# Kernel tuning notes

Measured on AMD Instinct MI355X. Metric: run time of the kernel, lower is better.

## Reference

```python
import jax, jax.numpy as jnp
import numpy as np

EPS = 1e-8
N = 1024          # number of points
C = 16            # channels per layer
RBF_LOW, RBF_HIGH, RBF_COUNT = 0.0, 3.5, 32


def _rand(key, shape, scale=0.1):
    return scale * jax.random.normal(key, shape, dtype=jnp.float32)


def setup_inputs() -> dict:
    key = jax.random.key(0)
    ks = jax.random.split(key, 20)
    R = RBF_COUNT
    return {
        'points':   jax.random.normal(ks[0], (N, 3), dtype=jnp.float32),
        # layer 1: 2 radial filters (0->0 and 0->1), output_dim = 1 input channel
        'l1_W1':    _rand(ks[1],  (2, R, R)),
        'l1_B1':    _rand(ks[2],  (2, R)),
        'l1_W2':    _rand(ks[3],  (2, R, 1)),
        'l1_B2':    _rand(ks[4],  (2, 1)),
        'l1_si0_w': _rand(ks[5],  (C, 1)),
        'l1_si0_b': _rand(ks[6],  (C,)),
        'l1_si1_w': _rand(ks[7],  (C, 1)),
        'l1_nl_b':  _rand(ks[8],  (C,)),
        # layer 2: 5 radial filters (0->0, 0->1, 1->0, 1->1 id, 1->1 levi-civita)
        'l2_W1':    _rand(ks[9],  (5, R, R)),
        'l2_B1':    _rand(ks[10], (5, R)),
        'l2_W2':    _rand(ks[11], (5, R, C)),
        'l2_B2':    _rand(ks[12], (5, C)),
        'l2_si0_w': _rand(ks[13], (C, 2 * C)),
        'l2_si0_b': _rand(ks[14], (C,)),
        'l2_si1_w': _rand(ks[15], (C, 3 * C)),
        'l2_nl_b':  _rand(ks[16], (C,)),
        # readout
        'fc_w':     _rand(ks[17], (C, 8)),
        'fc_b':     _rand(ks[18], (8,)),
    }


def _eijk():
    e = np.zeros((3, 3, 3), dtype=np.float32)
    e[0, 1, 2] = e[1, 2, 0] = e[2, 0, 1] = 1.0
    e[0, 2, 1] = e[2, 1, 0] = e[1, 0, 2] = -1.0
    return jnp.asarray(e)


def _norm_eps(x, axis, keepdims=False):
    # norm_with_epsilon: sqrt(max(sum(x^2), EPS))
    return jnp.sqrt(jnp.maximum(jnp.sum(x * x, axis=axis, keepdims=keepdims), EPS))


def _radial(rbf, w1, b1, w2, b2):
    # R(): two-layer relu MLP on rbf features -> [N, N, F]
    h = jax.nn.relu(rbf @ w1 + b1)
    return h @ w2 + b2


def _geometry(points):
    rij = points[:, None, :] - points[None, :, :]          # [N,N,3]
    ss = jnp.sum(rij * rij, axis=-1)                        # [N,N]
    mask0 = ss < EPS                                        # dij == 0 (diagonal)
    dij = jnp.where(mask0, 0.0, jnp.sqrt(jnp.where(mask0, 1.0, ss)))
    centers = jnp.linspace(RBF_LOW, RBF_HIGH, RBF_COUNT, dtype=jnp.float32)
    gamma = jnp.float32(RBF_COUNT / (RBF_HIGH - RBF_LOW))
    rbf = jnp.exp(-gamma * (dij[..., None] - centers) ** 2)  # [N,N,RBF]
    unit = rij / _norm_eps(rij, axis=-1, keepdims=True)       # unit_vectors
    return rbf, unit, mask0


def _F1(rad, unit, mask0):
    # F_1: mask radial where dij==0, multiply by unit vectors -> [N,N,F,3]
    mr = jnp.where(mask0[..., None], 0.0, rad)
    return mr[..., None] * unit[:, :, None, :]


def _nonlinearity(x0, x1, b1):
    # degree-0: pointwise elu; degree-1: norm nonlinearity x * elu(|x|+b)/|x|
    x0 = jax.nn.elu(x0)
    n = _norm_eps(x1, axis=-1)                              # [N,C]
    x1 = x1 * (jax.nn.elu(n + b1) / n)[..., None]
    return x0, x1


def reference(points, l1_W1, l1_B1, l1_W2, l1_B2, l1_si0_w, l1_si0_b, l1_si1_w,
              l1_nl_b, l2_W1, l2_B1, l2_W2, l2_B2, l2_si0_w, l2_si0_b, l2_si1_w,
              l2_nl_b, fc_w, fc_b):
    rbf, unit, mask0 = _geometry(points)
    eijk = _eijk().astype(points.dtype)
    n_pts = points.shape[0]
    x0 = jnp.ones((n_pts, 1, 1), dtype=points.dtype)        # degree-0 input [N,1,1]

    # ---- layer 1: only degree-0 input -> (0->0) and (0->1) filters ----
    r00 = _radial(rbf, l1_W1[0], l1_B1[0], l1_W2[0], l1_B2[0])
    out0 = jnp.einsum('abf,bfi->afi', r00, x0)              # filter_0
    F1a = _F1(_radial(rbf, l1_W1[1], l1_B1[1], l1_W2[1], l1_B2[1]), unit, mask0)
    out1 = jnp.einsum('abfi,bf->afi', F1a, x0[..., 0])
    x0 = jnp.einsum('afi,gf->agi', out0, l1_si0_w) + l1_si0_b[:, None]
    x1 = jnp.einsum('afi,gf->agi', out1, l1_si1_w)
    x0, x1 = _nonlinearity(x0, x1, l1_nl_b)                 # [N,C,1], [N,C,3]

    # ---- layer 2: degree-0 and degree-1 inputs -> 5 filters ----
    rads = [_radial(rbf, l2_W1[i], l2_B1[i], l2_W2[i], l2_B2[i]) for i in range(5)]
    c00 = jnp.einsum('abf,bfi->afi', rads[0], x0)                          # 0x0->0
    c01 = jnp.einsum('abfi,bf->afi', _F1(rads[1], unit, mask0), x0[..., 0])  # 0x1->1
    c10 = jnp.einsum('abfj,bfj->af', _F1(rads[2], unit, mask0), x1)[..., None]  # 1x1->0
    c11 = jnp.einsum('abf,bfi->afi', rads[3], x1)                          # 1x0->1
    c11x = jnp.einsum('ijk,abfj,bfk->afi', eijk, _F1(rads[4], unit, mask0), x1)  # 1x1->1
    cat0 = jnp.concatenate([c00, c10], axis=-2)             # [N,2C,1]
    cat1 = jnp.concatenate([c01, c11, c11x], axis=-2)       # [N,3C,3]
    x0 = jnp.einsum('afi,gf->agi', cat0, l2_si0_w) + l2_si0_b[:, None]
    x1 = jnp.einsum('afi,gf->agi', cat1, l2_si1_w)
    x0, x1 = _nonlinearity(x0, x1, l2_nl_b)

    # ---- readout: invariant degree-0 features, mean-pool over points ----
    g = jnp.mean(x0[..., 0], axis=0)                        # [C]
    return g @ fc_w + fc_b                                  # [num_classes]
```

## Files before the change

### kernel.cpp

```cpp
#include <hip/hip_runtime.h>
#include <hip/hip_bf16.h>
#include <math.h>

#define NP 1024
#define R 32
#define C 16
#define GAMMA (32.0f/3.5f)
#define DC (3.5f/31.0f)
#define GDC2 (64.0f/31.0f)
#define GDD  (112.0f/961.0f)
#define NBANK 32

typedef __attribute__((ext_vector_type(8))) short bf16x8;
typedef __attribute__((ext_vector_type(4))) float f32x4;

__device__ __forceinline__ short tobf(float x){
    __hip_bfloat16 h = __float2bfloat16(x);
    return __builtin_bit_cast(short, h);
}
__device__ __forceinline__ unsigned pack2bf(float a, float b){
    const unsigned lo = (unsigned short)tobf(a);
    const unsigned hi = (unsigned short)tobf(b);
    return lo | (hi << 16);
}
__device__ __forceinline__ float eluf(float x){ return x > 0.f ? x : expm1f(x); }

__device__ __forceinline__ f32x4 mfma16(bf16x8 a, bf16x8 b, f32x4 c){
    return __builtin_amdgcn_mfma_f32_16x16x32_bf16(a, b, c, 0, 0, 0);
}

template<int STRIDE>
__device__ __forceinline__ void load_bfrag(const float* __restrict__ src, int q, int n,
                                           bf16x8& w){
    #pragma unroll
    for (int jj = 0; jj < 8; jj++)
        w[jj] = tobf(src[(q*8+jj)*STRIDE + n]);
}

__device__ __forceinline__ bf16x8 rbf_frag(float d, float qd8, float c0q, float c1){
    const float t0 = d - qd8;
    float r = __expf(-GAMMA * t0 * t0);
    float M = __expf(GDC2 * d) * c0q;
    bf16x8 afrag;
    afrag[0] = tobf(r);
    #pragma unroll
    for (int jj = 1; jj < 8; jj++){
        r *= M;  M *= c1;
        afrag[jj] = tobf(r);
    }
    return afrag;
}

__global__ __launch_bounds__(256) void k_l1p(
    const float* __restrict__ points,
    const float* __restrict__ W1, const float* __restrict__ B1,
    const float* __restrict__ W2, const float* __restrict__ B2,
    const float* __restrict__ si0w, const float* __restrict__ si0b,
    const float* __restrict__ si1w, const float* __restrict__ nlb,
    float* __restrict__ xall, float* __restrict__ l1c,
    unsigned* __restrict__ cntL1)
{
    __shared__ float sW[4][8];
    __shared__ float sFin[8];
    __shared__ unsigned sAm;

    const int tid  = threadIdx.x;
    const int lane = tid & 63;
    const int wv   = tid >> 6;
    const int l16  = lane & 15;
    const int q    = lane >> 4;
    const int a    = blockIdx.x >> 1;
    const int half = blockIdx.x & 1;
    const float pax = points[a*3+0], pay = points[a*3+1], paz = points[a*3+2];
    const float qd8 = (float)(q*8) * DC;
    const float c0q = __expf(-GDD * (1.0f + 16.0f*(float)q));
    const float c1  = __expf(-2.0f * GDD);

    bf16x8 w1f[2][2];
    float  b1v[2][2], w2s[2], w2t[2];
    #pragma unroll
    for (int fi = 0; fi < 2; fi++)
        #pragma unroll
        for (int nt = 0; nt < 2; nt++){
            load_bfrag<R>(W1 + fi*R*R, q, nt*16 + l16, w1f[fi][nt]);
            b1v[fi][nt] = B1[fi*R + nt*16 + l16];
        }
    #pragma unroll
    for (int nt = 0; nt < 2; nt++){
        w2s[nt] = W2[nt*16 + l16];
        w2t[nt] = W2[R + nt*16 + l16];
    }

    float s0a[2] = {0.f, 0.f};
    float T[2][3] = {};
    float upx = 0.f, upy = 0.f, upz = 0.f;

    for (int bt = half*8; bt < half*8 + 8; bt++){
        const int bA = bt*64 + wv*16 + l16;
        const float rx = pax - points[bA*3+0];
        const float ry = pay - points[bA*3+1];
        const float rz = paz - points[bA*3+2];
        const float ss = rx*rx + ry*ry + rz*rz;
        const float inv = 1.0f / sqrtf(fmaxf(ss, 1e-8f));
        const float dij = ss * inv;
        const float ux = rx*inv, uy = ry*inv, uz = rz*inv;
        upx += ux; upy += uy; upz += uz;

        const bf16x8 afrag = rbf_frag(dij, qd8, c0q, c1);

        float uxr[4], uyr[4], uzr[4];
        #pragma unroll
        for (int r4 = 0; r4 < 4; r4++){
            const int sl = q*4 + r4;
            uxr[r4] = __shfl(ux, sl, 16);
            uyr[r4] = __shfl(uy, sl, 16);
            uzr[r4] = __shfl(uz, sl, 16);
        }

        #pragma unroll
        for (int nt = 0; nt < 2; nt++){
            f32x4 c = {b1v[0][nt], b1v[0][nt], b1v[0][nt], b1v[0][nt]};
            c = mfma16(afrag, w1f[0][nt], c);
            s0a[nt] += fmaxf(c[0],0.f)+fmaxf(c[1],0.f)+fmaxf(c[2],0.f)+fmaxf(c[3],0.f);
        }
        #pragma unroll
        for (int nt = 0; nt < 2; nt++){
            f32x4 c = {b1v[1][nt], b1v[1][nt], b1v[1][nt], b1v[1][nt]};
            c = mfma16(afrag, w1f[1][nt], c);
            #pragma unroll
            for (int r4 = 0; r4 < 4; r4++){
                const float h = fmaxf(c[r4], 0.f);
                T[nt][0] = fmaf(h, uxr[r4], T[nt][0]);
                T[nt][1] = fmaf(h, uyr[r4], T[nt][1]);
                T[nt][2] = fmaf(h, uzr[r4], T[nt][2]);
            }
        }
    }

    float v[7];
    v[0] = s0a[0]*w2s[0] + s0a[1]*w2s[1];
    #pragma unroll
    for (int i = 0; i < 3; i++)
        v[1+i] = T[0][i]*w2t[0] + T[1][i]*w2t[1];
    v[4] = upx; v[5] = upy; v[6] = upz;
    #pragma unroll
    for (int off = 32; off > 0; off >>= 1)
        #pragma unroll
        for (int k = 0; k < 7; k++)
            v[k] += __shfl_down(v[k], off, 64);
    if (lane == 0)
        #pragma unroll
        for (int k = 0; k < 7; k++) sW[wv][k] = v[k];
    __syncthreads();
    if (tid < 7)
        atomicAdd(&l1c[a*8 + tid], sW[0][tid] + sW[1][tid] + sW[2][tid] + sW[3][tid]);
    __syncthreads();
    if (tid == 0)
        sAm = (atomicAdd(&cntL1[a], 1u) == 1u) ? 1u : 0u;
    __syncthreads();
    if (sAm){
        if (tid < 7)
            sFin[tid] = __hip_atomic_load(&l1c[a*8 + tid], __ATOMIC_RELAXED,
                                          __HIP_MEMORY_SCOPE_AGENT);
        __syncthreads();
        if (tid < C){
            const int g = tid;
            const float o0  = sFin[0] + (float)NP * B2[0];
            const float o1x = sFin[1] + B2[1] * 0.25f * sFin[4];
            const float o1y = sFin[2] + B2[1] * 0.25f * sFin[5];
            const float o1z = sFin[3] + B2[1] * 0.25f * sFin[6];
            const float x0 = eluf(fmaf(o0, si0w[g], si0b[g]));
            const float w = si1w[g];
            const float tx = o1x*w, ty = o1y*w, tz = o1z*w;
            const float n = sqrtf(fmaxf(tx*tx + ty*ty + tz*tz, 1e-8f));
            const float sc = eluf(n + nlb[g]) / n;
            f32x4 st = {x0, tx*sc, ty*sc, tz*sc};
            *(f32x4*)&xall[(a*C + g)*4] = st;
        }
    }
}

__global__ __launch_bounds__(256) void k_l2r(
    const float* __restrict__ points,
    const float* __restrict__ W1, const float* __restrict__ B1,
    const float* __restrict__ W2, const float* __restrict__ B2,
    const float* __restrict__ xall,
    const float* __restrict__ si0w, const float* __restrict__ si0b,
    const float* __restrict__ fcw, const float* __restrict__ fcb,
    float* __restrict__ c00g, float* __restrict__ c10g,
    unsigned* __restrict__ cntA,
    float* __restrict__ partial, unsigned* __restrict__ cnt,
    float* __restrict__ out)
{
    __shared__ __align__(16) short sH[4][2][16*40];
    __shared__ float sRed[4][2][16];
    __shared__ float sP[16];
    __shared__ unsigned aDone, amLast;

    const int tid  = threadIdx.x;
    const int lane = tid & 63;
    const int wv   = tid >> 6;
    const int l16  = lane & 15;
    const int q    = lane >> 4;
    const int a    = blockIdx.x >> 1;
    const int half = blockIdx.x & 1;
    const float pax = points[a*3+0], pay = points[a*3+1], paz = points[a*3+2];
    const float qd8 = (float)(q*8) * DC;
    const float c0q = __expf(-GDD * (1.0f + 16.0f*(float)q));
    const float c1  = __expf(-2.0f * GDD);

    bf16x8 w1f[2][2], w2f[2];
    float  b1v[2][2], b2v[2];
    #pragma unroll
    for (int fi = 0; fi < 2; fi++){
        const int fx = (fi == 0) ? 0 : 2;
        #pragma unroll
        for (int nt = 0; nt < 2; nt++){
            load_bfrag<R>(W1 + fx*R*R, q, 2*l16 + nt, w1f[fi][nt]);
            b1v[fi][nt] = B1[fx*R + 2*l16 + nt];
        }
        load_bfrag<C>(W2 + fx*R*C, q, l16, w2f[fi]);
        b2v[fi] = B2[fx*C + l16];
    }

    float acc0 = 0.f, acc1 = 0.f;
    short* sH0 = sH[wv][0];
    short* sH1 = sH[wv][1];

    for (int bt = half*8; bt < half*8 + 8; bt++){
        const int bA = bt*64 + wv*16 + l16;
        const float rx = pax - points[bA*3+0];
        const float ry = pay - points[bA*3+1];
        const float rz = paz - points[bA*3+2];
        const float ss = rx*rx + ry*ry + rz*rz;
        const float inv = 1.0f / sqrtf(fmaxf(ss, 1e-8f));
        const float dij = ss * inv;
        const float ux = rx*inv, uy = ry*inv, uz = rz*inv;

        float uxr[4], uyr[4], uzr[4];
        #pragma unroll
        for (int r4 = 0; r4 < 4; r4++){
            const int sl = q*4 + r4;
            uxr[r4] = __shfl(ux, sl, 16);
            uyr[r4] = __shfl(uy, sl, 16);
            uzr[r4] = __shfl(uz, sl, 16);
        }

        const f32x4* xp = (const f32x4*)&xall[((bt*64 + wv*16 + q*4)*C + l16)*4];
        float x0v[4], udv[4];
        #pragma unroll
        for (int r4 = 0; r4 < 4; r4++){
            const f32x4 xv = xp[r4*C];
            x0v[r4] = xv[0];
            udv[r4] = uxr[r4]*xv[1] + uyr[r4]*xv[2] + uzr[r4]*xv[3];
        }

        const bf16x8 afrag = rbf_frag(dij, qd8, c0q, c1);

        #pragma unroll
        for (int fi = 0; fi < 2; fi++){
            f32x4 c0 = {b1v[fi][0], b1v[fi][0], b1v[fi][0], b1v[fi][0]};
            c0 = mfma16(afrag, w1f[fi][0], c0);
            f32x4 c1f = {b1v[fi][1], b1v[fi][1], b1v[fi][1], b1v[fi][1]};
            c1f = mfma16(afrag, w1f[fi][1], c1f);
            short* sHf = (fi == 0) ? sH0 : sH1;
            #pragma unroll
            for (int r4 = 0; r4 < 4; r4++){
                const unsigned p = pack2bf(fmaxf(c0[r4], 0.f), fmaxf(c1f[r4], 0.f));
                *(unsigned*)&sHf[(q*4+r4)*40 + 2*l16] = p;
            }
        }
        asm volatile("s_waitcnt lgkmcnt(0)" ::: "memory");

        {
            const bf16x8 hf = *(const bf16x8*)(sH0 + l16*40 + q*8);
            f32x4 d = {0.f, 0.f, 0.f, 0.f};
            d = mfma16(hf, w2f[0], d);
            #pragma unroll
            for (int r4 = 0; r4 < 4; r4++)
                acc0 = fmaf(d[r4] + b2v[0], x0v[r4], acc0);
        }
        {
            const bf16x8 hf = *(const bf16x8*)(sH1 + l16*40 + q*8);
            f32x4 d = {0.f, 0.f, 0.f, 0.f};
            d = mfma16(hf, w2f[1], d);
            #pragma unroll
            for (int r4 = 0; r4 < 4; r4++)
                acc1 = fmaf(d[r4] + b2v[1], udv[r4], acc1);
        }
    }

    acc0 += __shfl_down(acc0, 32, 64); acc0 += __shfl_down(acc0, 16, 64);
    acc1 += __shfl_down(acc1, 32, 64); acc1 += __shfl_down(acc1, 16, 64);
    if (lane < 16){ sRed[wv][0][lane] = acc0; sRed[wv][1][lane] = acc1; }
    __syncthreads();
    if (tid < 16)
        atomicAdd(&c00g[a*C + tid],
                  sRed[0][0][tid] + sRed[1][0][tid] + sRed[2][0][tid] + sRed[3][0][tid]);
    else if (tid < 32){
        const int f = tid - 16;
        atomicAdd(&c10g[a*C + f],
                  sRed[0][1][f] + sRed[1][1][f] + sRed[2][1][f] + sRed[3][1][f]);
    }
    __syncthreads();
    if (tid == 0)
        aDone = (atomicAdd(&cntA[a], 1u) == 1u) ? 1u : 0u;
    __syncthreads();

    if (aDone){
        if (tid < C){
            const int g = tid;
            float s = si0b[g];
            #pragma unroll
            for (int f = 0; f < C; f++){
                const float v0 = __hip_atomic_load(&c00g[a*C + f], __ATOMIC_RELAXED,
                                                   __HIP_MEMORY_SCOPE_AGENT);
                s = fmaf(v0, si0w[g*2*C + f], s);
            }
            #pragma unroll
            for (int f = 0; f < C; f++){
                const float v1 = __hip_atomic_load(&c10g[a*C + f], __ATOMIC_RELAXED,
                                                   __HIP_MEMORY_SCOPE_AGENT);
                s = fmaf(v1, si0w[g*2*C + C + f], s);
            }
            atomicAdd(&partial[(a & (NBANK-1))*C + g], eluf(s));
        }
        __syncthreads();
        if (tid == 0){
            amLast = 0u;
            const unsigned p1 = atomicAdd(&cnt[a & (NBANK-1)], 1u);
            if (p1 == (NP/NBANK) - 1u){
                const unsigned p2 = atomicAdd(&cnt[NBANK], 1u);
                if (p2 == NBANK - 1u) amLast = 1u;
            }
        }
        __syncthreads();
        if (amLast){
            if (tid < C){
                float v = 0.f;
                #pragma unroll
                for (int b = 0; b < NBANK; b++)
                    v += __hip_atomic_load(&partial[b*C + tid], __ATOMIC_RELAXED,
                                           __HIP_MEMORY_SCOPE_AGENT);
                sP[tid] = v;
            }
            __syncthreads();
            if (tid < 8){
                float s = fcb[tid];
                #pragma unroll
                for (int g = 0; g < C; g++)
                    s = fmaf(sP[g] * (1.0f / (float)NP), fcw[g*8 + tid], s);
                out[tid] = s;
            }
        }
    }
}

extern "C" void kernel_launch(void* const* d_in, const int* in_sizes, int n_in,
                              void* d_out, int out_size, void* d_ws, size_t ws_size,
                              hipStream_t stream)
{
    (void)in_sizes; (void)n_in; (void)out_size; (void)ws_size;
    const float* points   = (const float*)d_in[0];
    const float* l1_W1    = (const float*)d_in[1];
    const float* l1_B1    = (const float*)d_in[2];
    const float* l1_W2    = (const float*)d_in[3];
    const float* l1_B2    = (const float*)d_in[4];
    const float* l1_si0_w = (const float*)d_in[5];
    const float* l1_si0_b = (const float*)d_in[6];
    const float* l1_si1_w = (const float*)d_in[7];
    const float* l1_nl_b  = (const float*)d_in[8];
    const float* l2_W1    = (const float*)d_in[9];
    const float* l2_B1    = (const float*)d_in[10];
    const float* l2_W2    = (const float*)d_in[11];
    const float* l2_B2    = (const float*)d_in[12];
    const float* l2_si0_w = (const float*)d_in[13];
    const float* l2_si0_b = (const float*)d_in[14];
    const float* fc_w     = (const float*)d_in[17];
    const float* fc_b     = (const float*)d_in[18];

    float* ws        = (float*)d_ws;
    float* partial   = ws;
    unsigned* cnt    = (unsigned*)(partial + NBANK*C);
    unsigned* cntA   = cnt + 64;
    unsigned* cntL1  = cntA + NP;
    float* l1c       = (float*)(cntL1 + NP);
    float* c00g      = l1c + NP*8;
    float* c10g      = c00g + NP*C;
    float* xall      = c10g + NP*C;
    const size_t zeroBytes = (size_t)((char*)xall - (char*)ws);

    hipMemsetAsync(ws, 0, zeroBytes, stream);
    k_l1p<<<2*NP, 256, 0, stream>>>(points, l1_W1, l1_B1, l1_W2, l1_B2,
                                    l1_si0_w, l1_si0_b, l1_si1_w, l1_nl_b,
                                    xall, l1c, cntL1);
    k_l2r<<<2*NP, 256, 0, stream>>>(points, l2_W1, l2_B1, l2_W2, l2_B2,
                                    xall, l2_si0_w, l2_si0_b,
                                    fc_w, fc_b, c00g, c10g, cntA,
                                    partial, cnt, (float*)d_out);
}
```

Before: 143.8 us.

## Transpose MFMA operand order so outputs land per-lane, removing unit-vector shuffles

Swaps the A/B operands of the 16x16 MFMAs in both the layer-1 and layer-2 radial kernels, so each lane owns one neighbour point and four hidden or output features. The twelve per-iteration cross-lane shuffles of unit vectors go away, and W2 is folded into the layer-1 accumulation instead of being applied after the loop. In layer 2 the shared-memory staging layout is transposed to match, the xall loads become contiguous per lane, and the final reduction moves to 16-lane shuffles over four accumulators. The cost is more bias and weight registers and a different reduction pattern.

```diff
diff --git a/kernel.cpp b/kernel.cpp
--- a/kernel.cpp
+++ b/kernel.cpp
@@ -77,22 +77,27 @@
     const float c1  = __expf(-2.0f * GDD);
 
     bf16x8 w1f[2][2];
-    float  b1v[2][2], w2s[2], w2t[2];
+    float  b1r[2][2][4];
+    float  w2sr[2][4], w2tr[2][4];
     #pragma unroll
     for (int fi = 0; fi < 2; fi++)
         #pragma unroll
         for (int nt = 0; nt < 2; nt++){
             load_bfrag<R>(W1 + fi*R*R, q, nt*16 + l16, w1f[fi][nt]);
-            b1v[fi][nt] = B1[fi*R + nt*16 + l16];
-        }
-    #pragma unroll
-    for (int nt = 0; nt < 2; nt++){
-        w2s[nt] = W2[nt*16 + l16];
-        w2t[nt] = W2[R + nt*16 + l16];
-    }
-
-    float s0a[2] = {0.f, 0.f};
-    float T[2][3] = {};
+            #pragma unroll
+            for (int r4 = 0; r4 < 4; r4++)
+                b1r[fi][nt][r4] = B1[fi*R + nt*16 + q*4 + r4];
+        }
+    #pragma unroll
+    for (int nt = 0; nt < 2; nt++)
+        #pragma unroll
+        for (int r4 = 0; r4 < 4; r4++){
+            w2sr[nt][r4] = W2[nt*16 + q*4 + r4];
+            w2tr[nt][r4] = W2[R + nt*16 + q*4 + r4];
+        }
+
+    float sS = 0.f;
+    float tW[3] = {};
     float upx = 0.f, upy = 0.f, upz = 0.f;
 
     for (int bt = half*8; bt < half*8 + 8; bt++){
@@ -108,40 +113,30 @@
 
         const bf16x8 afrag = rbf_frag(dij, qd8, c0q, c1);
 
-        float uxr[4], uyr[4], uzr[4];
-        #pragma unroll
-        for (int r4 = 0; r4 < 4; r4++){
-            const int sl = q*4 + r4;
-            uxr[r4] = __shfl(ux, sl, 16);
-            uyr[r4] = __shfl(uy, sl, 16);
-            uzr[r4] = __shfl(uz, sl, 16);
-        }
-
         #pragma unroll
         for (int nt = 0; nt < 2; nt++){
-            f32x4 c = {b1v[0][nt], b1v[0][nt], b1v[0][nt], b1v[0][nt]};
-            c = mfma16(afrag, w1f[0][nt], c);
-            s0a[nt] += fmaxf(c[0],0.f)+fmaxf(c[1],0.f)+fmaxf(c[2],0.f)+fmaxf(c[3],0.f);
+            f32x4 c = {b1r[0][nt][0], b1r[0][nt][1], b1r[0][nt][2], b1r[0][nt][3]};
+            c = mfma16(w1f[0][nt], afrag, c);
+            #pragma unroll
+            for (int r4 = 0; r4 < 4; r4++)
+                sS = fmaf(fmaxf(c[r4], 0.f), w2sr[nt][r4], sS);
         }
         #pragma unroll
         for (int nt = 0; nt < 2; nt++){
-            f32x4 c = {b1v[1][nt], b1v[1][nt], b1v[1][nt], b1v[1][nt]};
-            c = mfma16(afrag, w1f[1][nt], c);
+            f32x4 c = {b1r[1][nt][0], b1r[1][nt][1], b1r[1][nt][2], b1r[1][nt][3]};
+            c = mfma16(w1f[1][nt], afrag, c);
             #pragma unroll
             for (int r4 = 0; r4 < 4; r4++){
-                const float h = fmaxf(c[r4], 0.f);
-                T[nt][0] = fmaf(h, uxr[r4], T[nt][0]);
-                T[nt][1] = fmaf(h, uyr[r4], T[nt][1]);
-                T[nt][2] = fmaf(h, uzr[r4], T[nt][2]);
+                const float hw = fmaxf(c[r4], 0.f) * w2tr[nt][r4];
+                tW[0] = fmaf(hw, ux, tW[0]);
+                tW[1] = fmaf(hw, uy, tW[1]);
+                tW[2] = fmaf(hw, uz, tW[2]);
             }
         }
     }
 
     float v[7];
-    v[0] = s0a[0]*w2s[0] + s0a[1]*w2s[1];
-    #pragma unroll
-    for (int i = 0; i < 3; i++)
-        v[1+i] = T[0][i]*w2t[0] + T[1][i]*w2t[1];
+    v[0] = sS; v[1] = tW[0]; v[2] = tW[1]; v[3] = tW[2];
     v[4] = upx; v[5] = upy; v[6] = upz;
     #pragma unroll
     for (int off = 32; off > 0; off >>= 1)
@@ -192,7 +187,7 @@
     float* __restrict__ partial, unsigned* __restrict__ cnt,
     float* __restrict__ out)
 {
-    __shared__ __align__(16) short sH[4][2][16*40];
+    __shared__ __align__(16) unsigned sHt[4][2][16*20];
     __shared__ float sRed[4][2][16];
     __shared__ float sP[16];
     __shared__ unsigned aDone, amLast;
@@ -210,22 +205,26 @@
     const float c1  = __expf(-2.0f * GDD);
 
     bf16x8 w1f[2][2], w2f[2];
-    float  b1v[2][2], b2v[2];
+    float  b1r[2][2][4], b2r[2][4];
     #pragma unroll
     for (int fi = 0; fi < 2; fi++){
         const int fx = (fi == 0) ? 0 : 2;
         #pragma unroll
         for (int nt = 0; nt < 2; nt++){
-            load_bfrag<R>(W1 + fx*R*R, q, 2*l16 + nt, w1f[fi][nt]);
-            b1v[fi][nt] = B1[fx*R + 2*l16 + nt];
+            load_bfrag<R>(W1 + fx*R*R, q, nt*16 + l16, w1f[fi][nt]);
+            #pragma unroll
+            for (int r4 = 0; r4 < 4; r4++)
+                b1r[fi][nt][r4] = B1[fx*R + nt*16 + q*4 + r4];
         }
         load_bfrag<C>(W2 + fx*R*C, q, l16, w2f[fi]);
-        b2v[fi] = B2[fx*C + l16];
-    }
-
-    float acc0 = 0.f, acc1 = 0.f;
-    short* sH0 = sH[wv][0];
-    short* sH1 = sH[wv][1];
+        #pragma unroll
+        for (int r4 = 0; r4 < 4; r4++)
+            b2r[fi][r4] = B2[fx*C + q*4 + r4];
+    }
+
+    float acc0[4] = {}, acc1[4] = {};
+    unsigned* sH0 = sHt[wv][0];
+    unsigned* sH1 = sHt[wv][1];
 
     for (int bt = half*8; bt < half*8 + 8; bt++){
         const int bA = bt*64 + wv*16 + l16;
@@ -237,62 +236,61 @@
         const float dij = ss * inv;
         const float ux = rx*inv, uy = ry*inv, uz = rz*inv;
 
-        float uxr[4], uyr[4], uzr[4];
+        const f32x4* xp = (const f32x4*)&xall[((bt*64 + wv*16 + l16)*C + q*4)*4];
+        float x0v[4], udv[4];
         #pragma unroll
         for (int r4 = 0; r4 < 4; r4++){
-            const int sl = q*4 + r4;
-            uxr[r4] = __shfl(ux, sl, 16);
-            uyr[r4] = __shfl(uy, sl, 16);
-            uzr[r4] = __shfl(uz, sl, 16);
-        }
-
-        const f32x4* xp = (const f32x4*)&xall[((bt*64 + wv*16 + q*4)*C + l16)*4];
-        float x0v[4], udv[4];
+            const f32x4 xv = xp[r4];
+            x0v[r4] = xv[0];
+            udv[r4] = ux*xv[1] + uy*xv[2] + uz*xv[3];
+        }
+
+        const bf16x8 afrag = rbf_frag(dij, qd8, c0q, c1);
+
+        #pragma unroll
+        for (int fi = 0; fi < 2; fi++){
+            unsigned* sHf = (fi == 0) ? sH0 : sH1;
+            #pragma unroll
+            for (int nt = 0; nt < 2; nt++){
+                f32x4 c = {b1r[fi][nt][0], b1r[fi][nt][1], b1r[fi][nt][2], b1r[fi][nt][3]};
+                c = mfma16(w1f[fi][nt], afrag, c);
+                #pragma unroll
+                for (int p = 0; p < 2; p++){
+                    const unsigned w = pack2bf(fmaxf(c[2*p], 0.f), fmaxf(c[2*p+1], 0.f));
+                    sHf[l16*20 + q*2 + 8*nt + p] = w;
+                }
+            }
+        }
+        asm volatile("s_waitcnt lgkmcnt(0)" ::: "memory");
+
+        #pragma unroll
+        for (int fi = 0; fi < 2; fi++){
+            const unsigned* sHf = (fi == 0) ? sH0 : sH1;
+            const bf16x8 hf = *(const bf16x8*)(sHf + l16*20 + q*4);
+            f32x4 d = {0.f, 0.f, 0.f, 0.f};
+            d = mfma16(w2f[fi], hf, d);
+            #pragma unroll
+            for (int r4 = 0; r4 < 4; r4++){
+                const float v = d[r4] + b2r[fi][r4];
+                if (fi == 0) acc0[r4] = fmaf(v, x0v[r4], acc0[r4]);
+                else         acc1[r4] = fmaf(v, udv[r4], acc1[r4]);
+            }
+        }
+    }
+
+    #pragma unroll
+    for (int off = 8; off > 0; off >>= 1)
         #pragma unroll
         for (int r4 = 0; r4 < 4; r4++){
-            const f32x4 xv = xp[r4*C];
-            x0v[r4] = xv[0];
-            udv[r4] = uxr[r4]*xv[1] + uyr[r4]*xv[2] + uzr[r4]*xv[3];
-        }
-
-        const bf16x8 afrag = rbf_frag(dij, qd8, c0q, c1);
-
-        #pragma unroll
-        for (int fi = 0; fi < 2; fi++){
-            f32x4 c0 = {b1v[fi][0], b1v[fi][0], b1v[fi][0], b1v[fi][0]};
-            c0 = mfma16(afrag, w1f[fi][0], c0);
-            f32x4 c1f = {b1v[fi][1], b1v[fi][1], b1v[fi][1], b1v[fi][1]};
-            c1f = mfma16(afrag, w1f[fi][1], c1f);
-            short* sHf = (fi == 0) ? sH0 : sH1;
-            #pragma unroll
-            for (int r4 = 0; r4 < 4; r4++){
-                const unsigned p = pack2bf(fmaxf(c0[r4], 0.f), fmaxf(c1f[r4], 0.f));
-                *(unsigned*)&sHf[(q*4+r4)*40 + 2*l16] = p;
-            }
-        }
-        asm volatile("s_waitcnt lgkmcnt(0)" ::: "memory");
-
-        {
-            const bf16x8 hf = *(const bf16x8*)(sH0 + l16*40 + q*8);
-            f32x4 d = {0.f, 0.f, 0.f, 0.f};
-            d = mfma16(hf, w2f[0], d);
-            #pragma unroll
-            for (int r4 = 0; r4 < 4; r4++)
-                acc0 = fmaf(d[r4] + b2v[0], x0v[r4], acc0);
-        }
-        {
-            const bf16x8 hf = *(const bf16x8*)(sH1 + l16*40 + q*8);
-            f32x4 d = {0.f, 0.f, 0.f, 0.f};
-            d = mfma16(hf, w2f[1], d);
-            #pragma unroll
-            for (int r4 = 0; r4 < 4; r4++)
-                acc1 = fmaf(d[r4] + b2v[1], udv[r4], acc1);
-        }
-    }
-
-    acc0 += __shfl_down(acc0, 32, 64); acc0 += __shfl_down(acc0, 16, 64);
-    acc1 += __shfl_down(acc1, 32, 64); acc1 += __shfl_down(acc1, 16, 64);
-    if (lane < 16){ sRed[wv][0][lane] = acc0; sRed[wv][1][lane] = acc1; }
+            acc0[r4] += __shfl_down(acc0[r4], off, 16);
+            acc1[r4] += __shfl_down(acc1[r4], off, 16);
+        }
+    if (l16 == 0)
+        #pragma unroll
+        for (int r4 = 0; r4 < 4; r4++){
+            sRed[wv][0][q*4 + r4] = acc0[r4];
+            sRed[wv][1][q*4 + r4] = acc1[r4];
+        }
     __syncthreads();
     if (tid < 16)
         atomicAdd(&c00g[a*C + tid],
```

Result: slower. 162.4 us (+12.9%).
